# Kernel tuning notes

Measured on AMD Instinct MI355X. Metric: run time of the kernel, lower is better.

## Reference

```python
import jax, jax.numpy as jnp
import numpy as np

B, N, C, NC = 16, 49, 512, 12  # batch, spatial tokens, channels, num AU classes
EPS = 1e-5


def bn(h, axes):
    # torch BatchNorm (training mode, gamma=1, beta=0): biased batch stats
    m = h.mean(axes, keepdims=True)
    v = h.var(axes, keepdims=True)
    return (h - m) * jax.lax.rsqrt(v + EPS)


def cross_attn(y, x, qw, qb, kw, kb, vw, vb):
    # CrossAttn: q from y, k/v from x; attention over the token (N) axis
    q = y @ qw.T + qb            # (..., N, C//2)
    k = x @ kw.T + kb
    v = x @ vw.T + vb            # (..., N, C)
    scale = (C // 2) ** -0.5
    attn = jax.nn.softmax(jnp.einsum('...ij,...kj->...ik', q, k) * scale, axis=-1)
    return attn @ v


def _gnn_block(x, edge, A, Bm, E, U, V):
    # One ME-GraphAU GCN message-passing block.
    # x: (B, NC, C) node feats; edge: (B, NC*NC, C), edge (i,j) stored at i*NC+j
    b = x.shape[0]
    Vix = x @ A.T   # gathered at end node j of each edge
    Vjx = x @ Bm.T  # gathered at start node i of each edge
    msg = (Vjx[:, :, None, :] + Vix[:, None, :, :]).reshape(b, NC * NC, C) + edge @ E.T
    edge = edge + jax.nn.relu(bn(msg, (0, 2)))              # bne: per-edge-slot stats
    e = jax.nn.sigmoid(edge).reshape(b, NC, NC, C)
    e = jax.nn.softmax(e, axis=2)                            # softmax over target j
    Ujx = x @ V.T                                            # start-node features
    agg = (e * Ujx[:, :, None, :]).sum(axis=1) / NC          # sum over source i -> node j
    xn = x @ U.T + agg
    x = jax.nn.relu(x + bn(xn, (0, 2)))                      # bnv: per-class stats
    return x, edge


def _forward(x, cls_w, cls_b, attn_qw, attn_qb, attn_kw, attn_kb, attn_vw, attn_vb,
             ep_w, ep_b, gnn_w, mlp_w1, mlp_b1, mlp_w2, mlp_b2, mlp_w3, mlp_b3,
             final_w, final_b):
    b = x.shape[0]
    # per-class LinearBlocks, batched: (B, NC, N, C)
    h = jnp.einsum('bnc,koc->bkno', x, cls_w) + cls_b[None, :, None, :]
    f_u = jax.nn.relu(bn(h, (0, 2)))           # each class has its own BN over (B, N)
    f_v = f_u.mean(-2)                          # (B, NC, C)

    # GEM edge extractor
    g = jnp.broadcast_to(x[:, None], (b, NC, N, C))
    feat = cross_attn(f_u, g, attn_qw[0], attn_qb[0], attn_kw[0], attn_kb[0], attn_vw[0], attn_vb[0])
    # feat_end[i*NC+j] = feat[i]; feat_start[i*NC+j] = feat[j]
    feat_end = jnp.broadcast_to(feat[:, :, None], (b, NC, NC, N, C)).reshape(b, NC * NC, N, C)
    feat_start = jnp.broadcast_to(feat[:, None, :], (b, NC, NC, N, C)).reshape(b, NC * NC, N, C)
    feat2 = cross_attn(feat_start, feat_end, attn_qw[1], attn_qb[1], attn_kw[1], attn_kb[1], attn_vw[1], attn_vb[1])
    edge = bn(feat2 @ ep_w.T + ep_b, (0, 2, 3))  # BatchNorm2d(NC*NC): stats over (B, N, C)
    f_e = edge.mean(-2)                           # (B, NC*NC, C)

    # two GCN message-passing blocks
    U1, V1, A1, B1, E1, U2, V2, A2, B2, E2 = gnn_w
    f_v, f_e = _gnn_block(f_v, f_e, A1, B1, E1, U1, V1)
    f_v, f_e = _gnn_block(f_v, f_e, A2, B2, E2, U2, V2)

    # vectorized pairwise class-link head (feed_type='vertex+edge'), pairs i<j in loop order
    iu, ju = np.triu_indices(NC, 1)
    edges = jnp.concatenate([f_e[:, iu * NC + ju], f_e[:, ju * NC + iu]], axis=-1)  # (B, 66, 2C)
    nodes = jnp.concatenate([f_v[:, iu], f_v[:, ju]], axis=-1)                       # (B, 66, 2C)

    def mlp(z, i):
        z = jax.nn.relu(z @ mlp_w1[i].T + mlp_b1[i])
        z = jax.nn.relu(z @ mlp_w2[i].T + mlp_b2[i])
        return z @ mlp_w3[i].T + mlp_b3[i]

    ed = mlp(edges, 0)
    nd = mlp(nodes, 1)
    return jnp.concatenate([ed, nd], axis=-1) @ final_w.T + final_b  # (B, 66, 4)


def setup_inputs() -> dict:
    key = jax.random.key(0)
    ks = jax.random.split(key, 12)

    def w(k, shape, fan_in):
        return jax.random.normal(k, shape, jnp.float32) * (2.0 / fan_in) ** 0.5

    return dict(
        x=jax.random.normal(ks[0], (B, N, C), jnp.float32),
        cls_w=w(ks[1], (NC, C, C), C),          # per-class Linear (out, in)
        cls_b=jnp.zeros((NC, C), jnp.float32),
        attn_qw=w(ks[2], (2, C // 2, C), C),    # [0]=FAM, [1]=ARM
        attn_qb=jnp.zeros((2, C // 2), jnp.float32),
        attn_kw=w(ks[3], (2, C // 2, C), C),
        attn_kb=jnp.zeros((2, C // 2), jnp.float32),
        attn_vw=w(ks[4], (2, C, C), C),
        attn_vb=jnp.zeros((2, C), jnp.float32),
        ep_w=w(ks[5], (C, C), C),               # GEM edge_proj
        ep_b=jnp.zeros((C,), jnp.float32),
        gnn_w=w(ks[6], (10, C, C), C),          # U1,V1,A1,B1,E1,U2,V2,A2,B2,E2 (no bias)
        mlp_w1=w(ks[7], (2, C, 2 * C), 2 * C),  # [0]=edge_fc_*, [1]=node_fc_*
        mlp_b1=jnp.zeros((2, C), jnp.float32),
        mlp_w2=w(ks[8], (2, C // 2, C), C),
        mlp_b2=jnp.zeros((2, C // 2), jnp.float32),
        mlp_w3=w(ks[9], (2, 4, C // 2), C // 2),
        mlp_b3=jnp.zeros((2, 4), jnp.float32),
        final_w=w(ks[10], (4, 8), 8),
        final_b=jnp.zeros((4,), jnp.float32),
    )


def reference(x, cls_w, cls_b, attn_qw, attn_qb, attn_kw, attn_kb, attn_vw, attn_vb,
              ep_w, ep_b, gnn_w, mlp_w1, mlp_b1, mlp_w2, mlp_b2, mlp_w3, mlp_b3,
              final_w, final_b):
    return _forward(x, cls_w, cls_b, attn_qw, attn_qb, attn_kw, attn_kb, attn_vw, attn_vb,
                    ep_w, ep_b, gnn_w, mlp_w1, mlp_b1, mlp_w2, mlp_b2, mlp_w3, mlp_b3,
                    final_w, final_b)
```

## Files before the change

kernel.cpp:

```cpp
#include <hip/hip_runtime.h>

#define BN_EPS 1e-5f

typedef float f32x4 __attribute__((ext_vector_type(4)));
typedef short s16x8 __attribute__((ext_vector_type(8)));

__device__ __forceinline__ short f2bf(float f) {
    unsigned u = __builtin_bit_cast(unsigned, f);
    u = (u + 0x7fffu + ((u >> 16) & 1u)) >> 16;
    return (short)u;
}

__global__ __launch_bounds__(256) void cvt_bf16_kernel(
    const float* __restrict__ src, short* __restrict__ dst, int n8)
{
    int idx = blockIdx.x * 256 + threadIdx.x;
    if (idx >= n8) return;
    const float4* s4 = reinterpret_cast<const float4*>(src) + (size_t)idx * 2;
    float4 a = s4[0], b = s4[1];
    s16x8 v;
    v[0] = f2bf(a.x); v[1] = f2bf(a.y); v[2] = f2bf(a.z); v[3] = f2bf(a.w);
    v[4] = f2bf(b.x); v[5] = f2bf(b.y); v[6] = f2bf(b.z); v[7] = f2bf(b.w);
    reinterpret_cast<s16x8*>(dst)[idx] = v;
}

template<int OMODE>
__global__ __launch_bounds__(256) void mfma_linear_kernel(
    const short* __restrict__ X, int Xstride,
    const short* __restrict__ W, int Wstride,
    const float* __restrict__ bias, int bstride,
    void* __restrict__ Yv, int Ystride,
    int R, int Cin, int Cout, int relu)
{
    const int mat = blockIdx.z;
    X += (size_t)mat * Xstride;
    W += (size_t)mat * Wstride;
    const float* bp = bias ? bias + mat * bstride : nullptr;
    float* Yf = (float*)Yv + (size_t)mat * Ystride;
    short* Ys = (short*)Yv + (size_t)mat * Ystride;

    const int r0 = blockIdx.y * 64;
    const int o0 = blockIdx.x * 64;

    __shared__ short As[64 * 40];
    __shared__ short Bs[64 * 40];

    const int tid = threadIdx.x;
    const int lane = tid & 63;
    const int wave = tid >> 6;
    const int wr = wave >> 1, wc = wave & 1;
    const int l15 = lane & 15;
    const int lk = lane >> 4;

    const int trow = tid >> 2;
    const int tseg = (tid & 3) * 8;

    f32x4 acc[2][2] = {};

    const int arow = r0 + trow;
    const bool aok = arow < R;
    const short* xrow = X + (size_t)arow * Cin + tseg;
    const short* wrow = W + (size_t)(o0 + trow) * Cin + tseg;

    for (int k0 = 0; k0 < Cin; k0 += 32) {
        s16x8 av = {};
        if (aok) av = *reinterpret_cast<const s16x8*>(xrow + k0);
        s16x8 bv = *reinterpret_cast<const s16x8*>(wrow + k0);
        *reinterpret_cast<s16x8*>(&As[trow * 40 + tseg]) = av;
        *reinterpret_cast<s16x8*>(&Bs[trow * 40 + tseg]) = bv;
        __syncthreads();

        s16x8 af[2], bf[2];
        #pragma unroll
        for (int mi = 0; mi < 2; mi++)
            af[mi] = *reinterpret_cast<const s16x8*>(&As[(wr * 32 + mi * 16 + l15) * 40 + lk * 8]);
        #pragma unroll
        for (int ni = 0; ni < 2; ni++)
            bf[ni] = *reinterpret_cast<const s16x8*>(&Bs[(wc * 32 + ni * 16 + l15) * 40 + lk * 8]);
        #pragma unroll
        for (int mi = 0; mi < 2; mi++)
            #pragma unroll
            for (int ni = 0; ni < 2; ni++)
                acc[mi][ni] = __builtin_amdgcn_mfma_f32_16x16x32_bf16(af[mi], bf[ni], acc[mi][ni], 0, 0, 0);
        __syncthreads();
    }

    #pragma unroll
    for (int mi = 0; mi < 2; mi++) {
        #pragma unroll
        for (int ni = 0; ni < 2; ni++) {
            int col = o0 + wc * 32 + ni * 16 + l15;
            int row0 = r0 + wr * 32 + mi * 16 + lk * 4;
            float bb = bp ? bp[col] : 0.f;
            #pragma unroll
            for (int r = 0; r < 4; r++) {
                int row = row0 + r;
                if (row < R) {
                    float v = acc[mi][ni][r] + bb;
                    if (relu) v = fmaxf(v, 0.f);
                    if (OMODE == 0) {
                        Yf[(size_t)row * Cout + col] = v;
                    } else if (OMODE == 1) {
                        Ys[(size_t)row * Cout + col] = f2bf(v);
                    } else {
                        int t = row / 49, n = row - t * 49;
                        Ys[((size_t)t * 512 + col) * 64 + n] = f2bf(v);
                    }
                }
            }
        }
    }
}

__global__ __launch_bounds__(256) void bn1_partial_kernel(
    const float* __restrict__ h, float* __restrict__ bsum, float* __restrict__ bsq)
{
    int k = blockIdx.x;
    int part = blockIdx.y;
    int tid = threadIdx.x;
    #pragma unroll
    for (int half = 0; half < 2; half++) {
        int o = tid + half * 256;
        const float* base = h + (size_t)k * 401408 + (size_t)part * 98 * 512 + o;
        float s = 0.f, sq = 0.f;
        #pragma unroll 7
        for (int bn = 0; bn < 98; bn++) {
            float v = base[bn * 512];
            s += v; sq += v * v;
        }
        atomicAdd(&bsum[k * 512 + o], s);
        atomicAdd(&bsq[k * 512 + o], sq);
    }
}

__global__ __launch_bounds__(256) void fu_fv_kernel(
    const float* __restrict__ h, const float* __restrict__ bsum,
    const float* __restrict__ bsq, short* __restrict__ fu_bf,
    float* __restrict__ f_v, short* __restrict__ fv_bf)
{
    int b = blockIdx.x;
    int k = blockIdx.y;
    int tid = threadIdx.x;
    #pragma unroll
    for (int half = 0; half < 2; half++) {
        int o = tid + half * 256;
        float mu = bsum[k * 512 + o] * (1.f / 784.f);
        float var = bsq[k * 512 + o] * (1.f / 784.f) - mu * mu;
        float rs = rsqrtf(var + BN_EPS);
        const float* base = h + (size_t)(k * 16 + b) * 49 * 512 + o;
        short* obase = fu_bf + (size_t)(k * 16 + b) * 49 * 512 + o;
        float acc = 0.f;
        #pragma unroll 7
        for (int n = 0; n < 49; n++) {
            float v = (base[n * 512] - mu) * rs;
            v = fmaxf(v, 0.f);
            obase[n * 512] = f2bf(v);
            acc += v;
        }
        float fvv = acc * (1.f / 49.f);
        f_v[(b * 12 + k) * 512 + o] = fvv;
        fv_bf[(b * 12 + k) * 512 + o] = f2bf(fvv);
    }
}

__global__ __launch_bounds__(256) void attn1_kernel(
    const float* __restrict__ q1,
    const float* __restrict__ k1,
    const float* __restrict__ v1,
    short* __restrict__ feat)
{
    int b = blockIdx.x;
    int k = blockIdx.y;
    __shared__ float ks[49 * 260];
    __shared__ float Pt[49 * 56];
    int tid = threadIdx.x;
    const float* kb = k1 + b * 49 * 256;
    for (int e = tid; e < 49 * 256; e += 256) ks[(e >> 8) * 260 + (e & 255)] = kb[e];
    __syncthreads();
    const float* qb = q1 + (k * 16 + b) * 49 * 256;
    for (int e = tid; e < 49 * 49; e += 256) {
        int qi = e / 49, kj = e - qi * 49;
        const float4* q4 = reinterpret_cast<const float4*>(qb + qi * 256);
        const float4* k4 = reinterpret_cast<const float4*>(ks + kj * 260);
        float s = 0.f;
        #pragma unroll 8
        for (int d = 0; d < 64; d++) {
            float4 a = q4[d], c = k4[d];
            s += a.x * c.x + a.y * c.y + a.z * c.z + a.w * c.w;
        }
        Pt[kj * 56 + qi] = s * 0.0625f;
    }
    __syncthreads();
    if (tid < 196) {
        int qi = tid >> 2, sub = tid & 3;
        float ev[13];
        float m = -1e30f;
        #pragma unroll 13
        for (int t = 0; t < 13; t++) {
            int j = sub + t * 4;
            ev[t] = (j < 49) ? Pt[j * 56 + qi] : -1e30f;
            m = fmaxf(m, ev[t]);
        }
        m = fmaxf(m, __shfl_xor(m, 1));
        m = fmaxf(m, __shfl_xor(m, 2));
        float s = 0.f;
        #pragma unroll 13
        for (int t = 0; t < 13; t++) { ev[t] = __expf(ev[t] - m); s += ev[t]; }
        s += __shfl_xor(s, 1);
        s += __shfl_xor(s, 2);
        float inv = 1.f / s;
        #pragma unroll 13
        for (int t = 0; t < 13; t++) {
            int j = sub + t * 4;
            if (j < 49) Pt[j * 56 + qi] = ev[t] * inv;
        }
    }
    __syncthreads();
    const float* vb = v1 + b * 49 * 512;
    short* fb = feat + (size_t)(k * 16 + b) * 49 * 512;
    for (int qc = 0; qc < 49; qc += 8) {
        int nq = 49 - qc; if (nq > 8) nq = 8;
        float a0[8] = {}, a1[8] = {};
        for (int kj = 0; kj < 49; kj++) {
            float v0 = vb[kj * 512 + tid];
            float v1v = vb[kj * 512 + 256 + tid];
            const float4* pr = reinterpret_cast<const float4*>(&Pt[kj * 56 + qc]);
            float4 p0 = pr[0], p1 = pr[1];
            a0[0] += p0.x * v0; a1[0] += p0.x * v1v;
            a0[1] += p0.y * v0; a1[1] += p0.y * v1v;
            a0[2] += p0.z * v0; a1[2] += p0.z * v1v;
            a0[3] += p0.w * v0; a1[3] += p0.w * v1v;
            a0[4] += p1.x * v0; a1[4] += p1.x * v1v;
            a0[5] += p1.y * v0; a1[5] += p1.y * v1v;
            a0[6] += p1.z * v0; a1[6] += p1.z * v1v;
            a0[7] += p1.w * v0; a1[7] += p1.w * v1v;
        }
        #pragma unroll 8
        for (int u = 0; u < 8; u++) {
            if (u < nq) {
                fb[(qc + u) * 512 + tid] = f2bf(a0[u]);
                fb[(qc + u) * 512 + 256 + tid] = f2bf(a1[u]);
            }
        }
    }
}

__global__ __launch_bounds__(256) void attn2_mfma_kernel(
    const short* __restrict__ q2,
    const short* __restrict__ k2,
    const short* __restrict__ w2vT,
    const float* __restrict__ ep_b,
    float* __restrict__ fe_raw,
    float* __restrict__ stats)
{
    const int b = blockIdx.x, i = blockIdx.y;
    __shared__ short Vs[512 * 64];
    __shared__ float S[64 * 68];
    __shared__ short P[64 * 88];
    const int tid = threadIdx.x;
    const int lane = tid & 63, w = tid >> 6;
    const int l15 = lane & 15, lk = lane >> 4;

    {
        const float4* src = reinterpret_cast<const float4*>(w2vT + (size_t)((i * 16 + b) * 512) * 64);
        float4* dst = reinterpret_cast<float4*>(Vs);
        #pragma unroll
        for (int it = 0; it < 16; it++) {
            int c = tid + it * 256;
            int ch = c >> 3, c8 = c & 7;
            dst[(ch << 3) | (c8 ^ (ch & 7))] = src[c];
        }
        for (int idx = tid; idx < 64 * 88; idx += 256) P[idx] = 0;
    }
    const short* kb = k2 + (size_t)((i * 16 + b) * 49) * 256;
    __syncthreads();

    for (int j = 0; j < 12; j++) {
        const short* qb = q2 + (size_t)((j * 16 + b) * 49) * 256;
        {
            int qrow = w * 16 + l15; if (qrow > 48) qrow = 48;
            f32x4 sacc[4] = {};
            #pragma unroll
            for (int ks = 0; ks < 8; ks++) {
                s16x8 aq = *reinterpret_cast<const s16x8*>(qb + (size_t)qrow * 256 + ks * 32 + lk * 8);
                #pragma unroll
                for (int ni = 0; ni < 4; ni++) {
                    int krow = ni * 16 + l15; if (krow > 48) krow = 48;
                    s16x8 bk = *reinterpret_cast<const s16x8*>(kb + (size_t)krow * 256 + ks * 32 + lk * 8);
                    sacc[ni] = __builtin_amdgcn_mfma_f32_16x16x32_bf16(aq, bk, sacc[ni], 0, 0, 0);
                }
            }
            #pragma unroll
            for (int ni = 0; ni < 4; ni++)
                #pragma unroll
                for (int r = 0; r < 4; r++)
                    S[(w * 16 + lk * 4 + r) * 68 + ni * 16 + l15] = sacc[ni][r] * 0.0625f;
        }
        __syncthreads();

        if (tid < 196) {
            int qi = tid >> 2, sub = tid & 3;
            float ev[13];
            float m = -1e30f;
            #pragma unroll 13
            for (int t = 0; t < 13; t++) {
                int kk = sub + t * 4;
                ev[t] = (kk < 49) ? S[qi * 68 + kk] : -1e30f;
                m = fmaxf(m, ev[t]);
            }
            m = fmaxf(m, __shfl_xor(m, 1));
            m = fmaxf(m, __shfl_xor(m, 2));
            float s = 0.f;
            #pragma unroll 13
            for (int t = 0; t < 13; t++) { ev[t] = __expf(ev[t] - m); s += ev[t]; }
            s += __shfl_xor(s, 1);
            s += __shfl_xor(s, 2);
            float inv = 1.f / s;
            #pragma unroll 13
            for (int t = 0; t < 13; t++) {
                int kk = sub + t * 4;
                if (kk < 49) P[qi * 88 + kk] = f2bf(ev[t] * inv);
            }
        }
        __syncthreads();

        const int slot = i * 12 + j;
        float tot = 0.f, csq = 0.f;
        #pragma unroll
        for (int half = 0; half < 2; half++) {
            const int cb = half * 256 + w * 64;
            f32x4 pac[4][4] = {};
            #pragma unroll
            for (int ks = 0; ks < 2; ks++) {
                s16x8 bv[4];
                #pragma unroll
                for (int ni = 0; ni < 4; ni++) {
                    int ch = cb + ni * 16 + l15;
                    int boff = ((ch * 64 + ks * 32 + lk * 8) * 2) ^ ((ch & 7) << 4);
                    bv[ni] = *reinterpret_cast<const s16x8*>(reinterpret_cast<const char*>(Vs) + boff);
                }
                #pragma unroll
                for (int mi = 0; mi < 4; mi++) {
                    s16x8 ap = *reinterpret_cast<const s16x8*>(&P[(mi * 16 + l15) * 88 + ks * 32 + lk * 8]);
                    #pragma unroll
                    for (int ni = 0; ni < 4; ni++)
                        pac[mi][ni] = __builtin_amdgcn_mfma_f32_16x16x32_bf16(ap, bv[ni], pac[mi][ni], 0, 0, 0);
                }
            }
            #pragma unroll
            for (int ni = 0; ni < 4; ni++) {
                int col = cb + ni * 16 + l15;
                float bias = ep_b[col];
                float cs = 0.f;
                #pragma unroll
                for (int mi = 0; mi < 4; mi++) {
                    #pragma unroll
                    for (int r = 0; r < 4; r++) {
                        int row = mi * 16 + lk * 4 + r;
                        if (row < 49) {
                            float sv = pac[mi][ni][r] + bias;
                            cs += sv; csq += sv * sv;
                        }
                    }
                }
                tot += cs;
                cs += __shfl_xor(cs, 16);
                cs += __shfl_xor(cs, 32);
                if (lk == 0)
                    fe_raw[((size_t)b * 144 + slot) * 512 + col] = cs * (1.f / 49.f);
            }
        }
        tot += __shfl_xor(tot, 1);  tot += __shfl_xor(tot, 2);  tot += __shfl_xor(tot, 4);
        tot += __shfl_xor(tot, 8);  tot += __shfl_xor(tot, 16); tot += __shfl_xor(tot, 32);
        csq += __shfl_xor(csq, 1);  csq += __shfl_xor(csq, 2);  csq += __shfl_xor(csq, 4);
        csq += __shfl_xor(csq, 8);  csq += __shfl_xor(csq, 16); csq += __shfl_xor(csq, 32);
        if (lane == 0) {
            atomicAdd(&stats[slot * 2], tot);
            atomicAdd(&stats[slot * 2 + 1], csq);
        }
    }
}

__global__ __launch_bounds__(256) void edge_fin_kernel(
    const float* __restrict__ stats, float* __restrict__ fe, short* __restrict__ fe_bf)
{
    int s = blockIdx.x;
    const float inv = 1.f / 401408.f;
    float mu = stats[s * 2] * inv;
    float var = stats[s * 2 + 1] * inv - mu * mu;
    float rs = rsqrtf(var + BN_EPS);
    int tid = threadIdx.x;
    for (int b = 0; b < 16; b++) {
        float* p = fe + (b * 144 + s) * 512;
        short* pb = fe_bf + (b * 144 + s) * 512;
        #pragma unroll
        for (int half = 0; half < 2; half++) {
            int c = tid + half * 256;
            float nv = (p[c] - mu) * rs;
            p[c] = nv;
            pb[c] = f2bf(nv);
        }
    }
}

__global__ __launch_bounds__(256) void gnn_edge_kernel(
    const float* __restrict__ nodeproj,
    const float* __restrict__ eE,
    float* __restrict__ fe, short* __restrict__ fe_bf)
{
    int s = blockIdx.x;
    int i = s / 12, j = s - i * 12;
    int tid = threadIdx.x;
    const float* Vix = nodeproj + 2 * 98304;
    const float* Vjx = nodeproj + 3 * 98304;
    __shared__ float red[256];
    float msg[32];
    float sum = 0.f, sq = 0.f;
    int idx = 0;
    for (int b = 0; b < 16; b++) {
        #pragma unroll
        for (int half = 0; half < 2; half++) {
            int c = tid + half * 256;
            float v = Vjx[(b * 12 + i) * 512 + c] + Vix[(b * 12 + j) * 512 + c]
                    + eE[(b * 144 + s) * 512 + c];
            msg[idx++] = v;
            sum += v; sq += v * v;
        }
    }
    red[tid] = sum; __syncthreads();
    for (int t = 128; t > 0; t >>= 1) { if (tid < t) red[tid] += red[tid + t]; __syncthreads(); }
    float tsum = red[0]; __syncthreads();
    red[tid] = sq; __syncthreads();
    for (int t = 128; t > 0; t >>= 1) { if (tid < t) red[tid] += red[tid + t]; __syncthreads(); }
    float tsq = red[0];
    float mu = tsum * (1.f / 8192.f);
    float var = tsq * (1.f / 8192.f) - mu * mu;
    float rs = rsqrtf(var + BN_EPS);
    idx = 0;
    for (int b = 0; b < 16; b++) {
        #pragma unroll
        for (int half = 0; half < 2; half++) {
            int c = tid + half * 256;
            int o = (b * 144 + s) * 512 + c;
            float v = fmaxf((msg[idx++] - mu) * rs, 0.f);
            float nv = fe[o] + v;
            fe[o] = nv;
            fe_bf[o] = f2bf(nv);
        }
    }
}

__global__ __launch_bounds__(256) void gnn_agg_kernel(
    const float* __restrict__ fe,
    const float* __restrict__ nodeproj,
    float* __restrict__ xn_agg)
{
    int b = blockIdx.x;
    int i = blockIdx.y;
    int tid = threadIdx.x;
    const float* Ujx = nodeproj + 98304;
    #pragma unroll
    for (int half = 0; half < 2; half++) {
        int c = tid + half * 256;
        float sg[12];
        float m = -1e30f;
        #pragma unroll
        for (int j = 0; j < 12; j++) {
            float e = fe[(b * 144 + i * 12 + j) * 512 + c];
            float sv = 1.f / (1.f + __expf(-e));
            sg[j] = sv;
            m = fmaxf(m, sv);
        }
        float ssum = 0.f;
        #pragma unroll
        for (int j = 0; j < 12; j++) { float evv = __expf(sg[j] - m); sg[j] = evv; ssum += evv; }
        float wgt = Ujx[(b * 12 + i) * 512 + c] / ssum;
        #pragma unroll
        for (int j = 0; j < 12; j++)
            atomicAdd(&xn_agg[(b * 12 + j) * 512 + c], sg[j] * wgt);
    }
}

__global__ __launch_bounds__(256) void gnn_node_kernel(
    const float* __restrict__ xn_agg, const float* __restrict__ nodeproj,
    float* __restrict__ fv, short* __restrict__ fv_bf)
{
    int k = blockIdx.x;
    int tid = threadIdx.x;
    const float* Ux = nodeproj;
    __shared__ float red[256];
    float vals[32];
    float sum = 0.f, sq = 0.f;
    int idx = 0;
    for (int b = 0; b < 16; b++) {
        #pragma unroll
        for (int half = 0; half < 2; half++) {
            int c = tid + half * 256;
            int o = (b * 12 + k) * 512 + c;
            float v = Ux[o] + xn_agg[o] * (1.f / 12.f);
            vals[idx++] = v;
            sum += v; sq += v * v;
        }
    }
    red[tid] = sum; __syncthreads();
    for (int t = 128; t > 0; t >>= 1) { if (tid < t) red[tid] += red[tid + t]; __syncthreads(); }
    float tsum = red[0]; __syncthreads();
    red[tid] = sq; __syncthreads();
    for (int t = 128; t > 0; t >>= 1) { if (tid < t) red[tid] += red[tid + t]; __syncthreads(); }
    float tsq = red[0];
    float mu = tsum * (1.f / 8192.f);
    float var = tsq * (1.f / 8192.f) - mu * mu;
    float rs = rsqrtf(var + BN_EPS);
    idx = 0;
    for (int b = 0; b < 16; b++) {
        #pragma unroll
        for (int half = 0; half < 2; half++) {
            int c = tid + half * 256;
            int o = (b * 12 + k) * 512 + c;
            float v = (vals[idx++] - mu) * rs;
            float nv = fmaxf(fv[o] + v, 0.f);
            fv[o] = nv;
            fv_bf[o] = f2bf(nv);
        }
    }
}

__global__ __launch_bounds__(256) void pair_gather_kernel(
    const float* __restrict__ fe, const float* __restrict__ fv, short* __restrict__ pairX)
{
    int p = blockIdx.x;
    int b = blockIdx.y;
    int tid = threadIdx.x;
    int i = 0, rem = p;
    while (rem >= 11 - i) { rem -= 11 - i; i++; }
    int j = i + 1 + rem;
    short* e_out = pairX + (size_t)(b * 66 + p) * 1024;
    short* n_out = pairX + (size_t)1056 * 1024 + (size_t)(b * 66 + p) * 1024;
    const float* fe_ij = fe + (b * 144 + i * 12 + j) * 512;
    const float* fe_ji = fe + (b * 144 + j * 12 + i) * 512;
    const float* fv_i = fv + (b * 12 + i) * 512;
    const float* fv_j = fv + (b * 12 + j) * 512;
    #pragma unroll
    for (int half = 0; half < 2; half++) {
        int c = tid + half * 256;
        e_out[c] = f2bf(fe_ij[c]);
        e_out[512 + c] = f2bf(fe_ji[c]);
        n_out[c] = f2bf(fv_i[c]);
        n_out[512 + c] = f2bf(fv_j[c]);
    }
}

__global__ __launch_bounds__(256) void mlp3_kernel(
    const float* __restrict__ X,
    const float* __restrict__ w3,
    const float* __restrict__ b3,
    float* __restrict__ Y)
{
    int idx = blockIdx.x * 256 + threadIdx.x;
    if (idx >= 8448) return;
    int o = idx & 3;
    int r = (idx >> 2) % 1056;
    int m = idx / (4 * 1056);
    const float* x = X + (m * 1056 + r) * 256;
    const float* w = w3 + (m * 4 + o) * 256;
    float s = b3[m * 4 + o];
    #pragma unroll 8
    for (int c = 0; c < 256; c++) s += x[c] * w[c];
    Y[idx] = s;
}

__global__ __launch_bounds__(256) void final_kernel(
    const float* __restrict__ mid3,
    const float* __restrict__ fw,
    const float* __restrict__ fb,
    float* __restrict__ out)
{
    int idx = blockIdx.x * 256 + threadIdx.x;
    if (idx >= 4224) return;
    int o = idx & 3;
    int r = idx >> 2;
    const float* ed = mid3 + r * 4;
    const float* nd = mid3 + 1056 * 4 + r * 4;
    float s = fb[o];
    #pragma unroll
    for (int q = 0; q < 4; q++) s += ed[q] * fw[o * 8 + q];
    #pragma unroll
    for (int q = 0; q < 4; q++) s += nd[q] * fw[o * 8 + 4 + q];
    out[idx] = s;
}

extern "C" void kernel_launch(void* const* d_in, const int* in_sizes, int n_in,
                              void* d_out, int out_size, void* d_ws, size_t ws_size,
                              hipStream_t stream)
{
    const float* x      = (const float*)d_in[0];
    const float* cls_w  = (const float*)d_in[1];
    const float* cls_b  = (const float*)d_in[2];
    const float* qw     = (const float*)d_in[3];
    const float* qb     = (const float*)d_in[4];
    const float* kw     = (const float*)d_in[5];
    const float* kb     = (const float*)d_in[6];
    const float* vw     = (const float*)d_in[7];
    const float* vb     = (const float*)d_in[8];
    const float* ep_w   = (const float*)d_in[9];
    const float* ep_b   = (const float*)d_in[10];
    const float* gnn_w  = (const float*)d_in[11];
    const float* mlp_w1 = (const float*)d_in[12];
    const float* mlp_b1 = (const float*)d_in[13];
    const float* mlp_w2 = (const float*)d_in[14];
    const float* mlp_b2 = (const float*)d_in[15];
    const float* mlp_w3 = (const float*)d_in[16];
    const float* mlp_b3 = (const float*)d_in[17];
    const float* fin_w  = (const float*)d_in[18];
    const float* fin_b  = (const float*)d_in[19];
    float* out = (float*)d_out;
    float* ws = (float*)d_ws;

    float* A      = ws;
    float* q1b    = A + 4816896;
    float* k1b    = q1b + 2408448;
    float* v1b    = k1b + 200704;
    float* Bb     = v1b + 401408;
    float* Cb     = Bb + 3145728;
    float* fv     = Cb + 2408448;
    float* fvbf_f = fv + 98304;
    float* bn1m   = fvbf_f + 49152;
    float* bn1r   = bn1m + 6144;
    float* fe     = bn1r + 6144;
    float* febf_f = fe + 1179648;
    float* stats  = febf_f + 589824;
    float* xbf_f  = stats + 288;
    float* cwbf_f = xbf_f + 200704;
    float* qwbf_f = cwbf_f + 1572864;
    float* kwbf_f = qwbf_f + 131072;
    float* vwbf_f = kwbf_f + 131072;
    float* ewbf_f = vwbf_f + 262144;
    float* gwbf_f = ewbf_f + 131072;
    float* m1bf_f = gwbf_f + 1310720;
    float* m2bf_f = m1bf_f + 524288;

    short* xbf   = (short*)xbf_f;
    short* cwbf  = (short*)cwbf_f;
    short* qwbf  = (short*)qwbf_f;
    short* kwbf  = (short*)kwbf_f;
    short* vwbf  = (short*)vwbf_f;
    short* ewbf  = (short*)ewbf_f;
    short* gwbf  = (short*)gwbf_f;
    short* m1wbf = (short*)m1bf_f;
    short* m2wbf = (short*)m2bf_f;

    short* fubf   = (short*)Cb;
    short* featbf = (short*)Bb;
    short* q2bf   = (short*)A;
    short* k2bf   = (short*)A + 2408448;
    short* v2bf   = (short*)Cb;
    short* w2vT   = (short*)Bb;
    short* fvbf   = (short*)fvbf_f;
    short* febf   = (short*)febf_f;

    float* nodeproj = Cb;
    float* eE       = Cb + 393216;
    float* xn       = Cb + 1572864;
    short* pairXbf  = (short*)Cb;
    short* mid1bf   = (short*)Cb + 2162688;
    float* mid2     = Cb + 1622016;
    float* mid3     = Cb + 2162688;

    auto cvt = [&](const float* s, short* d, int n) {
        int n8 = n / 8;
        cvt_bf16_kernel<<<(n8 + 255) / 256, 256, 0, stream>>>(s, d, n8);
    };
    cvt(x, xbf, 401408);
    cvt(cls_w, cwbf, 3145728);
    cvt(qw, qwbf, 262144);
    cvt(kw, kwbf, 262144);
    cvt(vw, vwbf, 524288);
    cvt(ep_w, ewbf, 262144);
    cvt(gnn_w, gwbf, 2621440);
    cvt(mlp_w1, m1wbf, 1048576);
    cvt(mlp_w2, m2wbf, 262144);

    mfma_linear_kernel<0><<<dim3(8, 13, 12), 256, 0, stream>>>(xbf, 0, cwbf, 262144, cls_b, 512,
                                                               A, 401408, 784, 512, 512, 0);
    hipMemsetAsync(bn1m, 0, 2 * 6144 * sizeof(float), stream);
    bn1_partial_kernel<<<dim3(12, 8), 256, 0, stream>>>(A, bn1m, bn1r);
    fu_fv_kernel<<<dim3(16, 12), 256, 0, stream>>>(A, bn1m, bn1r, fubf, fv, fvbf);
    mfma_linear_kernel<0><<<dim3(4, 147, 1), 256, 0, stream>>>(fubf, 0, qwbf, 0, qb, 0,
                                                               q1b, 0, 9408, 512, 256, 0);
    mfma_linear_kernel<0><<<dim3(4, 13, 1), 256, 0, stream>>>(xbf, 0, kwbf, 0, kb, 0,
                                                              k1b, 0, 784, 512, 256, 0);
    mfma_linear_kernel<0><<<dim3(8, 13, 1), 256, 0, stream>>>(xbf, 0, vwbf, 0, vb, 0,
                                                              v1b, 0, 784, 512, 512, 0);
    attn1_kernel<<<dim3(16, 12), 256, 0, stream>>>(q1b, k1b, v1b, featbf);
    mfma_linear_kernel<1><<<dim3(4, 147, 1), 256, 0, stream>>>(featbf, 0, qwbf + 131072, 0, qb + 256, 0,
                                                               q2bf, 0, 9408, 512, 256, 0);
    mfma_linear_kernel<1><<<dim3(4, 147, 1), 256, 0, stream>>>(featbf, 0, kwbf + 131072, 0, kb + 256, 0,
                                                               k2bf, 0, 9408, 512, 256, 0);
    mfma_linear_kernel<1><<<dim3(8, 147, 1), 256, 0, stream>>>(featbf, 0, vwbf + 262144, 0, vb + 512, 0,
                                                               v2bf, 0, 9408, 512, 512, 0);
    hipMemsetAsync(w2vT, 0, (size_t)12 * 16 * 512 * 64 * sizeof(short), stream);
    mfma_linear_kernel<2><<<dim3(8, 147, 1), 256, 0, stream>>>(v2bf, 0, ewbf, 0, nullptr, 0,
                                                               w2vT, 0, 9408, 512, 512, 0);
    hipMemsetAsync(stats, 0, 288 * sizeof(float), stream);
    attn2_mfma_kernel<<<dim3(16, 12), 256, 0, stream>>>(q2bf, k2bf, w2vT, ep_b, fe, stats);
    edge_fin_kernel<<<144, 256, 0, stream>>>(stats, fe, febf);

    for (int blk = 0; blk < 2; blk++) {
        const short* gw = gwbf + blk * 5 * 262144;
        mfma_linear_kernel<0><<<dim3(8, 3, 4), 256, 0, stream>>>(fvbf, 0, gw, 262144, nullptr, 0,
                                                                 nodeproj, 98304, 192, 512, 512, 0);
        mfma_linear_kernel<0><<<dim3(8, 36, 1), 256, 0, stream>>>(febf, 0, gw + 4 * 262144, 0, nullptr, 0,
                                                                  eE, 0, 2304, 512, 512, 0);
        gnn_edge_kernel<<<144, 256, 0, stream>>>(nodeproj, eE, fe, febf);
        hipMemsetAsync(xn, 0, 98304 * sizeof(float), stream);
        gnn_agg_kernel<<<dim3(16, 12), 256, 0, stream>>>(fe, nodeproj, xn);
        gnn_node_kernel<<<12, 256, 0, stream>>>(xn, nodeproj, fv, fvbf);
    }

    pair_gather_kernel<<<dim3(66, 16), 256, 0, stream>>>(fe, fv, pairXbf);
    mfma_linear_kernel<1><<<dim3(8, 17, 2), 256, 0, stream>>>(pairXbf, 1081344, m1wbf, 524288, mlp_b1, 512,
                                                              mid1bf, 540672, 1056, 1024, 512, 1);
    mfma_linear_kernel<0><<<dim3(4, 17, 2), 256, 0, stream>>>(mid1bf, 540672, m2wbf, 131072, mlp_b2, 256,
                                                              mid2, 270336, 1056, 512, 256, 1);
    mlp3_kernel<<<33, 256, 0, stream>>>(mid2, mlp_w3, mlp_b3, mid3);
    final_kernel<<<17, 256, 0, stream>>>(mid3, fin_w, fin_b, out);
}
```

Baseline: 497.3 us.

## Split attn2 over channel halves and merge bf16 conversion launches

The second cross-attention kernel gets a z grid dimension of 2. Each block loads and multiplies only 256 of the 512 value channels, which doubles the block count from 192 and halves shared memory per block. The cost is that each block recomputes the QK scores and softmax. Separately, the nine fp32-to-bf16 conversion launches are merged into one kernel that picks its source and destination by index range, removing per-launch overhead.

New measurement: 521.3 us. 4.8% more time.

```diff
diff --git a/kernel.cpp b/kernel.cpp
--- a/kernel.cpp
+++ b/kernel.cpp
@@ -11,17 +11,32 @@
     return (short)u;
 }
 
-__global__ __launch_bounds__(256) void cvt_bf16_kernel(
-    const float* __restrict__ src, short* __restrict__ dst, int n8)
+__global__ __launch_bounds__(256) void cvt_multi_kernel(
+    const float* __restrict__ s0, const float* __restrict__ s1, const float* __restrict__ s2,
+    const float* __restrict__ s3, const float* __restrict__ s4, const float* __restrict__ s5,
+    const float* __restrict__ s6, const float* __restrict__ s7, const float* __restrict__ s8,
+    short* __restrict__ d0, short* __restrict__ d1, short* __restrict__ d2,
+    short* __restrict__ d3, short* __restrict__ d4, short* __restrict__ d5,
+    short* __restrict__ d6, short* __restrict__ d7, short* __restrict__ d8)
 {
     int idx = blockIdx.x * 256 + threadIdx.x;
-    if (idx >= n8) return;
-    const float4* s4 = reinterpret_cast<const float4*>(src) + (size_t)idx * 2;
-    float4 a = s4[0], b = s4[1];
+    const float* src; short* dst; int local;
+    if      (idx <   50176) { src = s0; dst = d0; local = idx; }
+    else if (idx <  443392) { src = s1; dst = d1; local = idx -   50176; }
+    else if (idx <  476160) { src = s2; dst = d2; local = idx -  443392; }
+    else if (idx <  508928) { src = s3; dst = d3; local = idx -  476160; }
+    else if (idx <  574464) { src = s4; dst = d4; local = idx -  508928; }
+    else if (idx <  607232) { src = s5; dst = d5; local = idx -  574464; }
+    else if (idx <  934912) { src = s6; dst = d6; local = idx -  607232; }
+    else if (idx < 1065984) { src = s7; dst = d7; local = idx -  934912; }
+    else if (idx < 1098752) { src = s8; dst = d8; local = idx - 1065984; }
+    else return;
+    const float4* s4p = reinterpret_cast<const float4*>(src) + (size_t)local * 2;
+    float4 a = s4p[0], b = s4p[1];
     s16x8 v;
     v[0] = f2bf(a.x); v[1] = f2bf(a.y); v[2] = f2bf(a.z); v[3] = f2bf(a.w);
     v[4] = f2bf(b.x); v[5] = f2bf(b.y); v[6] = f2bf(b.z); v[7] = f2bf(b.w);
-    reinterpret_cast<s16x8*>(dst)[idx] = v;
+    reinterpret_cast<s16x8*>(dst)[local] = v;
 }
 
 template<int OMODE>
@@ -253,8 +268,8 @@
     float* __restrict__ fe_raw,
     float* __restrict__ stats)
 {
-    const int b = blockIdx.x, i = blockIdx.y;
-    __shared__ short Vs[512 * 64];
+    const int b = blockIdx.x, i = blockIdx.y, z = blockIdx.z;
+    __shared__ short Vs[256 * 64];
     __shared__ float S[64 * 68];
     __shared__ short P[64 * 88];
     const int tid = threadIdx.x;
@@ -262,10 +277,11 @@
     const int l15 = lane & 15, lk = lane >> 4;
 
     {
-        const float4* src = reinterpret_cast<const float4*>(w2vT + (size_t)((i * 16 + b) * 512) * 64);
+        const float4* src = reinterpret_cast<const float4*>(
+            w2vT + ((size_t)(i * 16 + b) * 512 + z * 256) * 64);
         float4* dst = reinterpret_cast<float4*>(Vs);
         #pragma unroll
-        for (int it = 0; it < 16; it++) {
+        for (int it = 0; it < 8; it++) {
             int c = tid + it * 256;
             int ch = c >> 3, c8 = c & 7;
             dst[(ch << 3) | (c8 ^ (ch & 7))] = src[c];
@@ -326,17 +342,16 @@
 
         const int slot = i * 12 + j;
         float tot = 0.f, csq = 0.f;
-        #pragma unroll
-        for (int half = 0; half < 2; half++) {
-            const int cb = half * 256 + w * 64;
+        {
+            const int lbase = w * 64;
             f32x4 pac[4][4] = {};
             #pragma unroll
             for (int ks = 0; ks < 2; ks++) {
                 s16x8 bv[4];
                 #pragma unroll
                 for (int ni = 0; ni < 4; ni++) {
-                    int ch = cb + ni * 16 + l15;
-                    int boff = ((ch * 64 + ks * 32 + lk * 8) * 2) ^ ((ch & 7) << 4);
+                    int lch = lbase + ni * 16 + l15;
+                    int boff = ((lch * 64 + ks * 32 + lk * 8) * 2) ^ ((lch & 7) << 4);
                     bv[ni] = *reinterpret_cast<const s16x8*>(reinterpret_cast<const char*>(Vs) + boff);
                 }
                 #pragma unroll
@@ -349,7 +364,7 @@
             }
             #pragma unroll
             for (int ni = 0; ni < 4; ni++) {
-                int col = cb + ni * 16 + l15;
+                int col = z * 256 + lbase + ni * 16 + l15;
                 float bias = ep_b[col];
                 float cs = 0.f;
                 #pragma unroll
@@ -666,19 +681,9 @@
     float* mid2     = Cb + 1622016;
     float* mid3     = Cb + 2162688;
 
-    auto cvt = [&](const float* s, short* d, int n) {
-        int n8 = n / 8;
-        cvt_bf16_kernel<<<(n8 + 255) / 256, 256, 0, stream>>>(s, d, n8);
-    };
-    cvt(x, xbf, 401408);
-    cvt(cls_w, cwbf, 3145728);
-    cvt(qw, qwbf, 262144);
-    cvt(kw, kwbf, 262144);
-    cvt(vw, vwbf, 524288);
-    cvt(ep_w, ewbf, 262144);
-    cvt(gnn_w, gwbf, 2621440);
-    cvt(mlp_w1, m1wbf, 1048576);
-    cvt(mlp_w2, m2wbf, 262144);
+    cvt_multi_kernel<<<4293, 256, 0, stream>>>(
+        x, cls_w, qw, kw, vw, ep_w, gnn_w, mlp_w1, mlp_w2,
+        xbf, cwbf, qwbf, kwbf, vwbf, ewbf, gwbf, m1wbf, m2wbf);
 
     mfma_linear_kernel<0><<<dim3(8, 13, 12), 256, 0, stream>>>(xbf, 0, cwbf, 262144, cls_b, 512,
                                                                A, 401408, 784, 512, 512, 0);
@@ -702,7 +707,7 @@
     mfma_linear_kernel<2><<<dim3(8, 147, 1), 256, 0, stream>>>(v2bf, 0, ewbf, 0, nullptr, 0,
                                                                w2vT, 0, 9408, 512, 512, 0);
     hipMemsetAsync(stats, 0, 288 * sizeof(float), stream);
-    attn2_mfma_kernel<<<dim3(16, 12), 256, 0, stream>>>(q2bf, k2bf, w2vT, ep_b, fe, stats);
+    attn2_mfma_kernel<<<dim3(16, 12, 2), 256, 0, stream>>>(q2bf, k2bf, w2vT, ep_b, fe, stats);
     edge_fin_kernel<<<144, 256, 0, stream>>>(stats, fe, febf);
 
     for (int blk = 0; blk < 2; blk++) {
```
